# Optimization experiments

Measured on AMD Instinct MI355X. Metric: run time of the kernel, lower is better.

Reference implementation:

```python
import math
import jax, jax.numpy as jnp
import numpy as np

B, T, D, H = 2, 2048, 1024, 16
N_LAYERS = 24


def get_slopes(n):
    def pow2(n):
        start = 2 ** (-2 ** (-(math.log2(n) - 3)))
        return [start * start ** i for i in range(n)]
    if math.log2(n).is_integer():
        return pow2(n)
    c = 2 ** math.floor(math.log2(n))
    return pow2(c) + get_slopes(2 * c)[0::2][: n - c]


def setup_inputs() -> dict:
    key = jax.random.key(0)
    ks = jax.random.split(key, 5)
    x = jax.random.normal(ks[0], (B, T, D), dtype=jnp.float32)
    Wq = 0.02 * jax.random.normal(ks[1], (D, D), dtype=jnp.float32)
    Wk = 0.02 * jax.random.normal(ks[2], (D, D), dtype=jnp.float32)
    Wv = 0.02 * jax.random.normal(ks[3], (D, D), dtype=jnp.float32)
    Wo = (0.02 / math.sqrt(2 * N_LAYERS)) * jax.random.normal(ks[4], (D, D), dtype=jnp.float32)
    z = jnp.zeros((D,), dtype=jnp.float32)
    return {"x": x, "Wq": Wq, "bq": z, "Wk": Wk, "bk": z, "Wv": Wv, "bv": z, "Wo": Wo, "bo": z}


def reference(x, Wq, bq, Wk, bk, Wv, bv, Wo, bo):
    Bb, Tt, C = x.shape
    hd = C // H
    # QKV projections -> (B, H, T, hd)
    q = (x @ Wq + bq).reshape(Bb, Tt, H, hd).transpose(0, 2, 1, 3)
    k = (x @ Wk + bk).reshape(Bb, Tt, H, hd).transpose(0, 2, 1, 3)
    v = (x @ Wv + bv).reshape(Bb, Tt, H, hd).transpose(0, 2, 1, 3)
    # scaled dot-product scores (B, H, T, T)
    attn = jnp.einsum('bhqd,bhkd->bhqk', q, k) / jnp.sqrt(jnp.asarray(hd, x.dtype))
    # ALiBi bias: module uses only last row of the relative-position matrix,
    # broadcast over query positions: -slope_h * (T-1 - j), shape (1, H, 1, T)
    slopes = jnp.asarray(get_slopes(H), dtype=x.dtype)
    alibi = -slopes[None, :, None, None] * (Tt - 1 - jnp.arange(Tt, dtype=x.dtype))[None, None, None, :]
    attn = attn + alibi
    # causal mask
    causal = jnp.tril(jnp.ones((Tt, Tt), dtype=bool))[None, None, :, :]
    attn = jnp.where(causal, attn, jnp.finfo(x.dtype).min)
    p = jax.nn.softmax(attn, axis=-1)
    out = jnp.einsum('bhqk,bhkd->bqhd', p, v).reshape(Bb, Tt, C)
    return out @ Wo + bo
```

## Files before the change

kernel.cpp:

```cpp
#include <hip/hip_runtime.h>
#include <hip/hip_bf16.h>

#define Bn 2
#define Tdim 2048
#define Ddim 1024
#define Hn 16
#define HD 64

typedef unsigned short u16;
typedef unsigned int u32;
typedef __attribute__((ext_vector_type(8))) __bf16 bf16x8;
typedef __attribute__((ext_vector_type(4))) float f32x4;
typedef __attribute__((ext_vector_type(16))) float f32x16;
typedef __attribute__((ext_vector_type(4))) u32 u32x4;

struct alignas(8) U16x4 { u16 x, y, z, w; };

__device__ __forceinline__ u16 f2bf(float f) {
  union { float f; u32 i; } v; v.f = f;
  u32 x = v.i;
  u32 r = (x + 0x7fffu + ((x >> 16) & 1u)) >> 16;
  return (u16)r;
}
__device__ __forceinline__ float bf2f(u16 u) {
  union { u32 i; float f; } v; v.i = ((u32)u) << 16; return v.f;
}
__device__ __forceinline__ u32 fbits(float f) {
  union { float f; u32 i; } v; v.f = f; return v.i;
}

__device__ __forceinline__ void cp16(const u16* g, u16* l) {
  __builtin_amdgcn_global_load_lds(
      (const __attribute__((address_space(1))) u32*)g,
      (__attribute__((address_space(3))) u32*)l, 16, 0, 0);
}

__device__ __forceinline__ f32x4 mfma16(bf16x8 a, bf16x8 b, f32x4 c) {
  return __builtin_amdgcn_mfma_f32_16x16x32_bf16(a, b, c, 0, 0, 0);
}
__device__ __forceinline__ f32x16 mfma32(bf16x8 a, bf16x8 b, f32x16 c) {
  return __builtin_amdgcn_mfma_f32_32x32x16_bf16(a, b, c, 0, 0, 0);
}

__global__ __launch_bounds__(256) void convert_x(const float* __restrict__ src,
                                                 u16* __restrict__ dst) {
  const int i = (blockIdx.x * 256 + threadIdx.x) * 8;
  u16 t[8];
#pragma unroll
  for (int j = 0; j < 8; j++) t[j] = f2bf(src[i + j]);
  *(bf16x8*)&dst[i] = *(const bf16x8*)t;
}

__global__ __launch_bounds__(256) void transpose_k(
    const float* __restrict__ s0, const float* __restrict__ s1,
    const float* __restrict__ s2, const float* __restrict__ s3,
    u16* __restrict__ dst) {
  const float* src = (blockIdx.z == 0) ? s0 : (blockIdx.z == 1) ? s1
                   : (blockIdx.z == 2) ? s2 : s3;
  u16* d = dst + (size_t)blockIdx.z * Ddim * Ddim;
  __shared__ u16 tile[32][33];
  const int tx = threadIdx.x, ty = threadIdx.y;
  const int x = blockIdx.x * 32 + tx;
  const int y0 = blockIdx.y * 32;
#pragma unroll
  for (int j = 0; j < 32; j += 8) tile[ty + j][tx] = f2bf(src[(size_t)(y0 + ty + j) * Ddim + x]);
  __syncthreads();
  const int xo = blockIdx.y * 32 + tx;
  const int yo0 = blockIdx.x * 32;
#pragma unroll
  for (int j = 0; j < 32; j += 8) d[(size_t)(yo0 + ty + j) * Ddim + xo] = tile[tx][ty + j];
}

__global__ __launch_bounds__(256, 2) void gemm_qkv(
    const u16* __restrict__ Xb, const u16* __restrict__ WT,
    const float* __restrict__ bq, const float* __restrict__ bk, const float* __restrict__ bv,
    u16* __restrict__ Q, u16* __restrict__ K, u16* __restrict__ Vt) {
  const int z = blockIdx.z;
  const u16* Wt = WT + (size_t)z * Ddim * Ddim;
  const float* bias = (z == 0) ? bq : (z == 1) ? bk : bv;
  u16* QK = (z == 0) ? Q : K;

  __shared__ alignas(16) u16 Alds[128 * 32];
  __shared__ alignas(16) u16 Blds[128 * 32];
  const int tid = threadIdx.x;
  const int w = tid >> 6, lane = tid & 63, ln = lane & 15, quad = lane >> 4;
  const int wm = (w >> 1) * 64, wn = (w & 1) * 64;
  const int tm = blockIdx.x * 128, tn = blockIdx.y * 128;

  f32x4 acc[4][4] = {};

  const int srow = tid >> 2, scol = (tid & 3) * 8;
  const u16* ag = Xb + (size_t)(tm + srow) * Ddim + scol;
  const u16* ag2 = ag + (size_t)64 * Ddim;
  const u16* bg = Wt + (size_t)(tn + srow) * Ddim + scol;
  const u16* bg2 = bg + (size_t)64 * Ddim;
  u16* al = &Alds[w * 512];
  u16* al2 = &Alds[2048 + w * 512];
  u16* bl = &Blds[w * 512];
  u16* bl2 = &Blds[2048 + w * 512];

  for (int k0 = 0; k0 < Ddim; k0 += 32) {
    __syncthreads();
    cp16(ag + k0, al);
    cp16(ag2 + k0, al2);
    cp16(bg + k0, bl);
    cp16(bg2 + k0, bl2);
    __syncthreads();
    bf16x8 af[4], bfr[4];
#pragma unroll
    for (int i = 0; i < 4; i++)
      af[i] = *(const bf16x8*)&Alds[(wm + i * 16 + ln) * 32 + quad * 8];
#pragma unroll
    for (int i = 0; i < 4; i++)
      bfr[i] = *(const bf16x8*)&Blds[(wn + i * 16 + ln) * 32 + quad * 8];
#pragma unroll
    for (int mi = 0; mi < 4; mi++)
#pragma unroll
      for (int ni = 0; ni < 4; ni++)
        acc[mi][ni] = mfma16(af[mi], bfr[ni], acc[mi][ni]);
  }

#pragma unroll
  for (int mi = 0; mi < 4; mi++) {
#pragma unroll
    for (int ni = 0; ni < 4; ni++) {
      const int gm0 = tm + wm + mi * 16 + quad * 4;
      const int gn = tn + wn + ni * 16 + ln;
      const float bv_ = bias[gn];
      const int hh = gn >> 6, dd = gn & 63;
      const int b0 = gm0 >> 11, t0 = gm0 & 2047;
      if (z < 2) {
        u16* p = QK + (((size_t)(b0 * Hn + hh) * Tdim) + t0) * HD + dd;
#pragma unroll
        for (int r = 0; r < 4; r++) p[r * HD] = f2bf(acc[mi][ni][r] + bv_);
      } else {
        U16x4 pk;
        pk.x = f2bf(acc[mi][ni][0] + bv_);
        pk.y = f2bf(acc[mi][ni][1] + bv_);
        pk.z = f2bf(acc[mi][ni][2] + bv_);
        pk.w = f2bf(acc[mi][ni][3] + bv_);
        *(U16x4*)&Vt[((size_t)(b0 * Hn + hh) * HD + dd) * Tdim + t0] = pk;
      }
    }
  }
}

#define KSTR 68
#define VSTR 132
#define L2E 1.44269504088896f
__global__ __launch_bounds__(256, 2) void attn_k(
    const u16* __restrict__ Q, const u16* __restrict__ K, const u16* __restrict__ Vt,
    u16* __restrict__ Op, float* __restrict__ lp) {
  __shared__ alignas(16) u16 Klds[128 * KSTR];
  __shared__ alignas(16) u16 Vtlds[64 * VSTR];

  const int bx = blockIdx.x;
  const int qb = 15 - (bx >> 1);
  const int s = bx & 1;
  const int bh = blockIdx.y;
  const int q0 = qb * 128;
  const int tid = threadIdx.x;
  const int w = tid >> 6, lane = tid & 63;
  const int qi = lane & 31, hf = lane >> 5;

  const u16* Qh = Q + (size_t)bh * Tdim * HD;
  const u16* Kh = K + (size_t)bh * Tdim * HD;
  const u16* Vh = Vt + (size_t)bh * HD * Tdim;
  const float slope = exp2f(-0.5f * (float)((bh & 15) + 1));

  const int nkt = qb + 1;
  const int h0 = (nkt + 1) >> 1;
  const int kt0 = s ? h0 : 0;
  const int kt1 = s ? nkt : h0;

  const int tg = q0 + w * 32 + qi;
  const float sl2 = slope * L2E;
  const float c1 = 0.125f * L2E;
  const float tt2 = (slope * (float)tg + 3.0f) * L2E;
  const float f4hf = (float)(4 * hf);
  float sg8[4], slm[4];
#pragma unroll
  for (int g = 0; g < 4; g++) sg8[g] = sl2 * (float)(8 * g);
#pragma unroll
  for (int m = 0; m < 4; m++) slm[m] = sl2 * (float)m;

  bf16x8 qf[4];
#pragma unroll
  for (int kc = 0; kc < 4; kc++)
    qf[kc] = *(const bf16x8*)&Qh[(size_t)tg * HD + kc * 16 + hf * 8];

  float lsum = 0.f;
  f32x16 oacc[2] = {};

  bf16x8 kreg[4], vreg[4];
  {
    const int kb = kt0 * 128;
#pragma unroll
    for (int c = 0; c < 4; c++) {
      const int e = c * 2048 + tid * 8;
      kreg[c] = *(const bf16x8*)&Kh[(size_t)(kb + (e >> 6)) * HD + (e & 63)];
      vreg[c] = *(const bf16x8*)&Vh[(size_t)(e >> 7) * Tdim + kb + (e & 127)];
    }
  }

  for (int kt = kt0; kt < kt1; kt++) {
    const int kb = kt * 128;
    __syncthreads();
#pragma unroll
    for (int c = 0; c < 4; c++) {
      const int e = c * 2048 + tid * 8;
      *(bf16x8*)&Klds[(e >> 6) * KSTR + (e & 63)] = kreg[c];
      *(bf16x8*)&Vtlds[(e >> 7) * VSTR + (e & 127)] = vreg[c];
    }
    __syncthreads();

    if (kt + 1 < kt1) {
      const int kb2 = kb + 128;
#pragma unroll
      for (int c = 0; c < 4; c++) {
        const int e = c * 2048 + tid * 8;
        kreg[c] = *(const bf16x8*)&Kh[(size_t)(kb2 + (e >> 6)) * HD + (e & 63)];
        vreg[c] = *(const bf16x8*)&Vh[(size_t)(e >> 7) * Tdim + kb2 + (e & 127)];
      }
    }

    f32x16 st[4] = {};
#pragma unroll
    for (int kc = 0; kc < 4; kc++) {
#pragma unroll
      for (int ni = 0; ni < 4; ni++) {
        bf16x8 kf = *(const bf16x8*)&Klds[(ni * 32 + qi) * KSTR + kc * 16 + hf * 8];
        st[ni] = mfma32(kf, qf[kc], st[ni]);
      }
    }

    const bool diag = (kt == nkt - 1);
    const float fkb = (float)kb + f4hf;
    bf16x8 pfrag[8];
#pragma unroll
    for (int ni = 0; ni < 4; ni++) {
      const float cni = __builtin_fmaf(sl2, fkb + (float)(32 * ni), -tt2);
      u32 pu[16];
      if (!diag) {
#pragma unroll
        for (int ri = 0; ri < 16; ri++) {
          const float e = __builtin_fmaf(st[ni][ri], c1, cni + sg8[ri >> 2] + slm[ri & 3]);
          const float p = __builtin_amdgcn_exp2f(e);
          lsum += p;
          pu[ri] = fbits(p) + 0x8000u;
        }
      } else {
#pragma unroll
        for (int ri = 0; ri < 16; ri++) {
          const int n = kb + ni * 32 + (ri & 3) + 8 * (ri >> 2) + 4 * hf;
          const float e = __builtin_fmaf(st[ni][ri], c1, cni + sg8[ri >> 2] + slm[ri & 3]);
          float p = __builtin_amdgcn_exp2f(e);
          if (n > tg) p = 0.f;
          lsum += p;
          pu[ri] = fbits(p) + 0x8000u;
        }
      }
      u32 pk[4][2];
#pragma unroll
      for (int g = 0; g < 4; g++) {
        pk[g][0] = __builtin_amdgcn_perm(pu[g * 4 + 1], pu[g * 4 + 0], 0x07060302u);
        pk[g][1] = __builtin_amdgcn_perm(pu[g * 4 + 3], pu[g * 4 + 2], 0x07060302u);
      }
#pragma unroll
      for (int a = 0; a < 2; a++) {
        const u32 snd0 = (hf == 0) ? pk[2 * a + 1][0] : pk[2 * a][0];
        const u32 snd1 = (hf == 0) ? pk[2 * a + 1][1] : pk[2 * a][1];
        const u32 rcv0 = (u32)__shfl_xor((int)snd0, 32);
        const u32 rcv1 = (u32)__shfl_xor((int)snd1, 32);
        u32x4 fr;
        fr.x = (hf == 0) ? pk[2 * a][0] : rcv0;
        fr.y = (hf == 0) ? pk[2 * a][1] : rcv1;
        fr.z = (hf == 0) ? rcv0 : pk[2 * a + 1][0];
        fr.w = (hf == 0) ? rcv1 : pk[2 * a + 1][1];
        pfrag[ni * 2 + a] = *(bf16x8*)&fr;
      }
    }

#pragma unroll
    for (int kf16 = 0; kf16 < 8; kf16++) {
#pragma unroll
      for (int nd = 0; nd < 2; nd++) {
        bf16x8 vf = *(const bf16x8*)&Vtlds[(nd * 32 + qi) * VSTR + kf16 * 16 + hf * 8];
        oacc[nd] = mfma32(pfrag[kf16], vf, oacc[nd]);
      }
    }
  }

  lsum += __shfl_xor(lsum, 32);
  if (hf == 0) lp[(size_t)s * 65536 + bh * Tdim + tg] = lsum;

  u16* Ob = Op + (size_t)s * (32u * Tdim * HD) + ((size_t)bh * Tdim) * HD;
#pragma unroll
  for (int nd = 0; nd < 2; nd++) {
#pragma unroll
    for (int ri = 0; ri < 16; ri++) {
      const int rq = (ri & 3) + 8 * (ri >> 2) + 4 * hf;
      const int t = q0 + w * 32 + rq;
      Ob[(size_t)t * HD + nd * 32 + qi] = f2bf(oacc[nd][ri]);
    }
  }
}

__global__ __launch_bounds__(256) void merge_k(const u16* __restrict__ Op,
                                               const float* __restrict__ lp,
                                               u16* __restrict__ AO) {
  const int i = blockIdx.x * 256 + threadIdx.x;
  const int d8 = i & 7;
  const int t = (i >> 3) & 2047;
  const int bh = i >> 14;
  const int b = bh >> 4, h = bh & 15;
  const float l = lp[bh * Tdim + t] + lp[65536 + bh * Tdim + t];
  const float inv = 1.0f / l;
  const size_t off = ((size_t)bh * Tdim + t) * HD + d8 * 8;
  const u16* O0 = Op + off;
  const u16* O1 = Op + (size_t)32 * Tdim * HD + off;
  u16 outv[8];
#pragma unroll
  for (int j = 0; j < 8; j++)
    outv[j] = f2bf((bf2f(O0[j]) + bf2f(O1[j])) * inv);
  *(bf16x8*)&AO[((size_t)(b * Tdim + t)) * Ddim + h * HD + d8 * 8] = *(const bf16x8*)outv;
}

__global__ __launch_bounds__(256, 2) void gemm_out(
    const u16* __restrict__ A, const u16* __restrict__ WoT, const float* __restrict__ bo,
    float* __restrict__ C) {
  __shared__ alignas(16) u16 Alds[128 * 32];
  __shared__ alignas(16) u16 Blds[128 * 32];
  const int tid = threadIdx.x;
  const int w = tid >> 6, lane = tid & 63, ln = lane & 15, quad = lane >> 4;
  const int wm = (w >> 1) * 64, wn = (w & 1) * 64;
  const int tm = blockIdx.x * 128, tn = blockIdx.y * 128;

  f32x4 acc[4][4] = {};

  const int srow = tid >> 2, scol = (tid & 3) * 8;
  const u16* ag = A + (size_t)(tm + srow) * Ddim + scol;
  const u16* ag2 = ag + (size_t)64 * Ddim;
  const u16* bg = WoT + (size_t)(tn + srow) * Ddim + scol;
  const u16* bg2 = bg + (size_t)64 * Ddim;
  u16* al = &Alds[w * 512];
  u16* al2 = &Alds[2048 + w * 512];
  u16* bl = &Blds[w * 512];
  u16* bl2 = &Blds[2048 + w * 512];

  for (int k0 = 0; k0 < Ddim; k0 += 32) {
    __syncthreads();
    cp16(ag + k0, al);
    cp16(ag2 + k0, al2);
    cp16(bg + k0, bl);
    cp16(bg2 + k0, bl2);
    __syncthreads();
    bf16x8 af[4], bfr[4];
#pragma unroll
    for (int i = 0; i < 4; i++)
      af[i] = *(const bf16x8*)&Alds[(wm + i * 16 + ln) * 32 + quad * 8];
#pragma unroll
    for (int i = 0; i < 4; i++)
      bfr[i] = *(const bf16x8*)&Blds[(wn + i * 16 + ln) * 32 + quad * 8];
#pragma unroll
    for (int mi = 0; mi < 4; mi++)
#pragma unroll
      for (int ni = 0; ni < 4; ni++)
        acc[mi][ni] = mfma16(af[mi], bfr[ni], acc[mi][ni]);
  }

#pragma unroll
  for (int mi = 0; mi < 4; mi++) {
#pragma unroll
    for (int ni = 0; ni < 4; ni++) {
      const int gm0 = tm + wm + mi * 16 + quad * 4;
      const int gn = tn + wn + ni * 16 + ln;
      const float bv_ = bo[gn];
#pragma unroll
      for (int r = 0; r < 4; r++)
        C[(size_t)(gm0 + r) * Ddim + gn] = acc[mi][ni][r] + bv_;
    }
  }
}

extern "C" void kernel_launch(void* const* d_in, const int* in_sizes, int n_in,
                              void* d_out, int out_size, void* d_ws, size_t ws_size,
                              hipStream_t stream) {
  (void)in_sizes; (void)n_in; (void)out_size; (void)ws_size;
  const float* x  = (const float*)d_in[0];
  const float* Wq = (const float*)d_in[1];
  const float* bq = (const float*)d_in[2];
  const float* Wk = (const float*)d_in[3];
  const float* bk = (const float*)d_in[4];
  const float* Wv = (const float*)d_in[5];
  const float* bv = (const float*)d_in[6];
  const float* Wo = (const float*)d_in[7];
  const float* bo = (const float*)d_in[8];

  char* ws = (char*)d_ws;
  const size_t MB = 1024 * 1024;
  u16* WT   = (u16*)(ws + 0 * MB);
  u16* Qb   = (u16*)(ws + 8 * MB);
  u16* Kb   = (u16*)(ws + 16 * MB);
  u16* Vtb  = (u16*)(ws + 24 * MB);
  u16* Xb   = (u16*)(ws + 32 * MB);
  u16* AO   = (u16*)(ws + 32 * MB);
  u16* Opart= (u16*)(ws + 40 * MB);
  float* lpart = (float*)(ws + 56 * MB);
  u16* WoT = WT + (size_t)3 * Ddim * Ddim;

  convert_x<<<dim3(2048), 256, 0, stream>>>(x, Xb);
  transpose_k<<<dim3(32, 32, 4), dim3(32, 8), 0, stream>>>(Wq, Wk, Wv, Wo, WT);

  gemm_qkv<<<dim3(32, 8, 3), 256, 0, stream>>>(Xb, WT, bq, bk, bv, Qb, Kb, Vtb);
  attn_k<<<dim3(32, 32), 256, 0, stream>>>(Qb, Kb, Vtb, Opart, lpart);
  merge_k<<<dim3(2048), 256, 0, stream>>>(Opart, lpart, AO);
  gemm_out<<<dim3(32, 8), 256, 0, stream>>>(AO, WoT, bo, (float*)d_out);
}
```

Baseline: 204.8 us.

## Fuse split-KV merge into output GEMM and restructure attention for occupancy

Drops the separate merge kernel: the output projection GEMM now reads both partial attention outputs and their row sums, normalises them on the fly, and writes the A tile into LDS itself. Its M tile shrinks to 64 and the grid doubles. The attention kernel drops the register prefetch of the next K/V tile, splits the score computation into two halves to cut live registers, and raises launch bounds to 4 blocks per CU. The aim is to save a kernel launch and the AO round trip and to gain occupancy, at the cost of exposed global-load latency in attention and redundant merge work repeated across the 8 N-tiles of the GEMM.

```diff
diff --git a/kernel.cpp b/kernel.cpp
--- a/kernel.cpp
+++ b/kernel.cpp
@@ -15,6 +15,9 @@
 typedef __attribute__((ext_vector_type(4))) u32 u32x4;
 
 struct alignas(8) U16x4 { u16 x, y, z, w; };
+struct alignas(16) U16x8 { u16 s[8]; };
+
+#define OSZ (32u * 2048u * 64u)
 
 __device__ __forceinline__ u16 f2bf(float f) {
   union { float f; u32 i; } v; v.f = f;
@@ -148,7 +151,7 @@
 #define KSTR 68
 #define VSTR 132
 #define L2E 1.44269504088896f
-__global__ __launch_bounds__(256, 2) void attn_k(
+__global__ __launch_bounds__(256, 4) void attn_k(
     const u16* __restrict__ Q, const u16* __restrict__ K, const u16* __restrict__ Vt,
     u16* __restrict__ Op, float* __restrict__ lp) {
   __shared__ alignas(16) u16 Klds[128 * KSTR];
@@ -192,101 +195,89 @@
   float lsum = 0.f;
   f32x16 oacc[2] = {};
 
-  bf16x8 kreg[4], vreg[4];
-  {
-    const int kb = kt0 * 128;
-#pragma unroll
-    for (int c = 0; c < 4; c++) {
-      const int e = c * 2048 + tid * 8;
-      kreg[c] = *(const bf16x8*)&Kh[(size_t)(kb + (e >> 6)) * HD + (e & 63)];
-      vreg[c] = *(const bf16x8*)&Vh[(size_t)(e >> 7) * Tdim + kb + (e & 127)];
-    }
-  }
-
   for (int kt = kt0; kt < kt1; kt++) {
     const int kb = kt * 128;
     __syncthreads();
-#pragma unroll
-    for (int c = 0; c < 4; c++) {
-      const int e = c * 2048 + tid * 8;
-      *(bf16x8*)&Klds[(e >> 6) * KSTR + (e & 63)] = kreg[c];
-      *(bf16x8*)&Vtlds[(e >> 7) * VSTR + (e & 127)] = vreg[c];
-    }
-    __syncthreads();
-
-    if (kt + 1 < kt1) {
-      const int kb2 = kb + 128;
+    {
+      bf16x8 kr[4], vr[4];
 #pragma unroll
       for (int c = 0; c < 4; c++) {
         const int e = c * 2048 + tid * 8;
-        kreg[c] = *(const bf16x8*)&Kh[(size_t)(kb2 + (e >> 6)) * HD + (e & 63)];
-        vreg[c] = *(const bf16x8*)&Vh[(size_t)(e >> 7) * Tdim + kb2 + (e & 127)];
+        kr[c] = *(const bf16x8*)&Kh[(size_t)(kb + (e >> 6)) * HD + (e & 63)];
+        vr[c] = *(const bf16x8*)&Vh[(size_t)(e >> 7) * Tdim + kb + (e & 127)];
       }
-    }
-
-    f32x16 st[4] = {};
-#pragma unroll
-    for (int kc = 0; kc < 4; kc++) {
-#pragma unroll
-      for (int ni = 0; ni < 4; ni++) {
-        bf16x8 kf = *(const bf16x8*)&Klds[(ni * 32 + qi) * KSTR + kc * 16 + hf * 8];
-        st[ni] = mfma32(kf, qf[kc], st[ni]);
+#pragma unroll
+      for (int c = 0; c < 4; c++) {
+        const int e = c * 2048 + tid * 8;
+        *(bf16x8*)&Klds[(e >> 6) * KSTR + (e & 63)] = kr[c];
+        *(bf16x8*)&Vtlds[(e >> 7) * VSTR + (e & 127)] = vr[c];
       }
     }
+    __syncthreads();
 
     const bool diag = (kt == nkt - 1);
     const float fkb = (float)kb + f4hf;
-    bf16x8 pfrag[8];
-#pragma unroll
-    for (int ni = 0; ni < 4; ni++) {
-      const float cni = __builtin_fmaf(sl2, fkb + (float)(32 * ni), -tt2);
-      u32 pu[16];
-      if (!diag) {
-#pragma unroll
-        for (int ri = 0; ri < 16; ri++) {
-          const float e = __builtin_fmaf(st[ni][ri], c1, cni + sg8[ri >> 2] + slm[ri & 3]);
-          const float p = __builtin_amdgcn_exp2f(e);
-          lsum += p;
-          pu[ri] = fbits(p) + 0x8000u;
-        }
-      } else {
-#pragma unroll
-        for (int ri = 0; ri < 16; ri++) {
-          const int n = kb + ni * 32 + (ri & 3) + 8 * (ri >> 2) + 4 * hf;
-          const float e = __builtin_fmaf(st[ni][ri], c1, cni + sg8[ri >> 2] + slm[ri & 3]);
-          float p = __builtin_amdgcn_exp2f(e);
-          if (n > tg) p = 0.f;
-          lsum += p;
-          pu[ri] = fbits(p) + 0x8000u;
+
+#pragma unroll
+    for (int half = 0; half < 2; half++) {
+      f32x16 st[2] = {};
+#pragma unroll
+      for (int kc = 0; kc < 4; kc++) {
+#pragma unroll
+        for (int j = 0; j < 2; j++) {
+          bf16x8 kf = *(const bf16x8*)&Klds[(half * 64 + j * 32 + qi) * KSTR + kc * 16 + hf * 8];
+          st[j] = mfma32(kf, qf[kc], st[j]);
         }
       }
-      u32 pk[4][2];
-#pragma unroll
-      for (int g = 0; g < 4; g++) {
-        pk[g][0] = __builtin_amdgcn_perm(pu[g * 4 + 1], pu[g * 4 + 0], 0x07060302u);
-        pk[g][1] = __builtin_amdgcn_perm(pu[g * 4 + 3], pu[g * 4 + 2], 0x07060302u);
-      }
-#pragma unroll
-      for (int a = 0; a < 2; a++) {
-        const u32 snd0 = (hf == 0) ? pk[2 * a + 1][0] : pk[2 * a][0];
-        const u32 snd1 = (hf == 0) ? pk[2 * a + 1][1] : pk[2 * a][1];
-        const u32 rcv0 = (u32)__shfl_xor((int)snd0, 32);
-        const u32 rcv1 = (u32)__shfl_xor((int)snd1, 32);
-        u32x4 fr;
-        fr.x = (hf == 0) ? pk[2 * a][0] : rcv0;
-        fr.y = (hf == 0) ? pk[2 * a][1] : rcv1;
-        fr.z = (hf == 0) ? rcv0 : pk[2 * a + 1][0];
-        fr.w = (hf == 0) ? rcv1 : pk[2 * a + 1][1];
-        pfrag[ni * 2 + a] = *(bf16x8*)&fr;
-      }
-    }
-
-#pragma unroll
-    for (int kf16 = 0; kf16 < 8; kf16++) {
-#pragma unroll
-      for (int nd = 0; nd < 2; nd++) {
-        bf16x8 vf = *(const bf16x8*)&Vtlds[(nd * 32 + qi) * VSTR + kf16 * 16 + hf * 8];
-        oacc[nd] = mfma32(pfrag[kf16], vf, oacc[nd]);
+#pragma unroll
+      for (int j = 0; j < 2; j++) {
+        const int ni = half * 2 + j;
+        const float cni = __builtin_fmaf(sl2, fkb + (float)(32 * ni), -tt2);
+        u32 pu[16];
+        if (!diag) {
+#pragma unroll
+          for (int ri = 0; ri < 16; ri++) {
+            const float e = __builtin_fmaf(st[j][ri], c1, cni + sg8[ri >> 2] + slm[ri & 3]);
+            const float p = __builtin_amdgcn_exp2f(e);
+            lsum += p;
+            pu[ri] = fbits(p) + 0x8000u;
+          }
+        } else {
+#pragma unroll
+          for (int ri = 0; ri < 16; ri++) {
+            const int n = kb + ni * 32 + (ri & 3) + 8 * (ri >> 2) + 4 * hf;
+            const float e = __builtin_fmaf(st[j][ri], c1, cni + sg8[ri >> 2] + slm[ri & 3]);
+            float p = __builtin_amdgcn_exp2f(e);
+            if (n > tg) p = 0.f;
+            lsum += p;
+            pu[ri] = fbits(p) + 0x8000u;
+          }
+        }
+        u32 pk[4][2];
+#pragma unroll
+        for (int g = 0; g < 4; g++) {
+          pk[g][0] = __builtin_amdgcn_perm(pu[g * 4 + 1], pu[g * 4 + 0], 0x07060302u);
+          pk[g][1] = __builtin_amdgcn_perm(pu[g * 4 + 3], pu[g * 4 + 2], 0x07060302u);
+        }
+#pragma unroll
+        for (int a = 0; a < 2; a++) {
+          const u32 snd0 = (hf == 0) ? pk[2 * a + 1][0] : pk[2 * a][0];
+          const u32 snd1 = (hf == 0) ? pk[2 * a + 1][1] : pk[2 * a][1];
+          const u32 rcv0 = (u32)__shfl_xor((int)snd0, 32);
+          const u32 rcv1 = (u32)__shfl_xor((int)snd1, 32);
+          u32x4 fr;
+          fr.x = (hf == 0) ? pk[2 * a][0] : rcv0;
+          fr.y = (hf == 0) ? pk[2 * a][1] : rcv1;
+          fr.z = (hf == 0) ? rcv0 : pk[2 * a + 1][0];
+          fr.w = (hf == 0) ? rcv1 : pk[2 * a + 1][1];
+          const bf16x8 pfrag = *(bf16x8*)&fr;
+          const int kf16 = ni * 2 + a;
+#pragma unroll
+          for (int nd = 0; nd < 2; nd++) {
+            bf16x8 vf = *(const bf16x8*)&Vtlds[(nd * 32 + qi) * VSTR + kf16 * 16 + hf * 8];
+            oacc[nd] = mfma32(pfrag, vf, oacc[nd]);
+          }
+        }
       }
     }
   }
@@ -294,7 +285,7 @@
   lsum += __shfl_xor(lsum, 32);
   if (hf == 0) lp[(size_t)s * 65536 + bh * Tdim + tg] = lsum;
 
-  u16* Ob = Op + (size_t)s * (32u * Tdim * HD) + ((size_t)bh * Tdim) * HD;
+  u16* Ob = Op + (size_t)s * OSZ + ((size_t)bh * Tdim) * HD;
 #pragma unroll
   for (int nd = 0; nd < 2; nd++) {
 #pragma unroll
@@ -306,71 +297,63 @@
   }
 }
 
-__global__ __launch_bounds__(256) void merge_k(const u16* __restrict__ Op,
-                                               const float* __restrict__ lp,
-                                               u16* __restrict__ AO) {
-  const int i = blockIdx.x * 256 + threadIdx.x;
-  const int d8 = i & 7;
-  const int t = (i >> 3) & 2047;
-  const int bh = i >> 14;
-  const int b = bh >> 4, h = bh & 15;
-  const float l = lp[bh * Tdim + t] + lp[65536 + bh * Tdim + t];
-  const float inv = 1.0f / l;
-  const size_t off = ((size_t)bh * Tdim + t) * HD + d8 * 8;
-  const u16* O0 = Op + off;
-  const u16* O1 = Op + (size_t)32 * Tdim * HD + off;
-  u16 outv[8];
-#pragma unroll
-  for (int j = 0; j < 8; j++)
-    outv[j] = f2bf((bf2f(O0[j]) + bf2f(O1[j])) * inv);
-  *(bf16x8*)&AO[((size_t)(b * Tdim + t)) * Ddim + h * HD + d8 * 8] = *(const bf16x8*)outv;
-}
-
-__global__ __launch_bounds__(256, 2) void gemm_out(
-    const u16* __restrict__ A, const u16* __restrict__ WoT, const float* __restrict__ bo,
+__global__ __launch_bounds__(256, 4) void gemm_out(
+    const u16* __restrict__ Op, const float* __restrict__ lp,
+    const u16* __restrict__ WoT, const float* __restrict__ bo,
     float* __restrict__ C) {
-  __shared__ alignas(16) u16 Alds[128 * 32];
+  __shared__ alignas(16) u16 Alds[64 * 32];
   __shared__ alignas(16) u16 Blds[128 * 32];
   const int tid = threadIdx.x;
   const int w = tid >> 6, lane = tid & 63, ln = lane & 15, quad = lane >> 4;
-  const int wm = (w >> 1) * 64, wn = (w & 1) * 64;
-  const int tm = blockIdx.x * 128, tn = blockIdx.y * 128;
-
-  f32x4 acc[4][4] = {};
+  const int wm = (w >> 1) * 32, wn = (w & 1) * 64;
+  const int tm = blockIdx.x * 64, tn = blockIdx.y * 128;
+
+  f32x4 acc[2][4] = {};
 
   const int srow = tid >> 2, scol = (tid & 3) * 8;
-  const u16* ag = A + (size_t)(tm + srow) * Ddim + scol;
-  const u16* ag2 = ag + (size_t)64 * Ddim;
+  const int arow = tm + srow;
+  const int t = arow & 2047, bb = arow >> 11;
   const u16* bg = WoT + (size_t)(tn + srow) * Ddim + scol;
   const u16* bg2 = bg + (size_t)64 * Ddim;
-  u16* al = &Alds[w * 512];
-  u16* al2 = &Alds[2048 + w * 512];
   u16* bl = &Blds[w * 512];
   u16* bl2 = &Blds[2048 + w * 512];
 
   for (int k0 = 0; k0 < Ddim; k0 += 32) {
     __syncthreads();
-    cp16(ag + k0, al);
-    cp16(ag2 + k0, al2);
     cp16(bg + k0, bl);
     cp16(bg2 + k0, bl2);
-    __syncthreads();
-    bf16x8 af[4], bfr[4];
-#pragma unroll
-    for (int i = 0; i < 4; i++)
+    {
+      const int col = k0 + scol;
+      const int h = col >> 6, d = col & 63;
+      const int bh = bb * 16 + h;
+      const float l = lp[bh * Tdim + t] + lp[65536 + bh * Tdim + t];
+      const float inv = 1.0f / l;
+      const size_t off = ((size_t)bh * Tdim + t) * HD + d;
+      U16x8 o0 = *(const U16x8*)&Op[off];
+      U16x8 o1 = *(const U16x8*)&Op[OSZ + off];
+      u16 tmp[8];
+#pragma unroll
+      for (int j = 0; j < 8; j++)
+        tmp[j] = f2bf((bf2f(o0.s[j]) + bf2f(o1.s[j])) * inv);
+      *(bf16x8*)&Alds[srow * 32 + scol] = *(const bf16x8*)tmp;
+    }
+    __syncthreads();
+    bf16x8 af[2], bfr[4];
+#pragma unroll
+    for (int i = 0; i < 2; i++)
       af[i] = *(const bf16x8*)&Alds[(wm + i * 16 + ln) * 32 + quad * 8];
 #pragma unroll
     for (int i = 0; i < 4; i++)
       bfr[i] = *(const bf16x8*)&Blds[(wn + i * 16 + ln) * 32 + quad * 8];
 #pragma unroll
-    for (int mi = 0; mi < 4; mi++)
+    for (int mi = 0; mi < 2; mi++)
 #pragma unroll
       for (int ni = 0; ni < 4; ni++)
         acc[mi][ni] = mfma16(af[mi], bfr[ni], acc[mi][ni]);
   }
 
 #pragma unroll
-  for (int mi = 0; mi < 4; mi++) {
+  for (int mi = 0; mi < 2; mi++) {
 #pragma unroll
     for (int ni = 0; ni < 4; ni++) {
       const int gm0 = tm + wm + mi * 16 + quad * 4;
@@ -404,7 +387,6 @@
   u16* Kb   = (u16*)(ws + 16 * MB);
   u16* Vtb  = (u16*)(ws + 24 * MB);
   u16* Xb   = (u16*)(ws + 32 * MB);
-  u16* AO   = (u16*)(ws + 32 * MB);
   u16* Opart= (u16*)(ws + 40 * MB);
   float* lpart = (float*)(ws + 56 * MB);
   u16* WoT = WT + (size_t)3 * Ddim * Ddim;
@@ -414,6 +396,5 @@
 
   gemm_qkv<<<dim3(32, 8, 3), 256, 0, stream>>>(Xb, WT, bq, bk, bv, Qb, Kb, Vtb);
   attn_k<<<dim3(32, 32), 256, 0, stream>>>(Qb, Kb, Vtb, Opart, lpart);
-  merge_k<<<dim3(2048), 256, 0, stream>>>(Opart, lpart, AO);
-  gemm_out<<<dim3(32, 8), 256, 0, stream>>>(AO, WoT, bo, (float*)d_out);
-}
+  gemm_out<<<dim3(64, 8), 256, 0, stream>>>(Opart, lpart, WoT, bo, (float*)d_out);
+}
```

After: 232.1 us. 13.3% more time.
